# Optimization experiments

Hardware: AMD Instinct MI355X
Metric: run time of the kernel (lower is better)

Reference implementation:

```python
import jax, jax.numpy as jnp
import numpy as np
from jax.ops import segment_sum

N_NODES = 50000
N_EDGES = 800000
D = 128
N_LAYERS = 3
N_GRAPHS = 256


def setup_inputs() -> dict:
    key = jax.random.key(0)
    k1, k2, k3, k4, k5, k6 = jax.random.split(key, 6)
    feats = jax.random.normal(k1, (N_NODES, D), dtype=jnp.float32)
    src = jax.random.randint(k2, (N_EDGES,), 0, N_NODES)
    dst = jax.random.randint(k3, (N_EDGES,), 0, N_NODES)
    graph_ids = jnp.sort(jax.random.randint(k4, (N_NODES,), 0, N_GRAPHS))
    W = jax.random.normal(k5, (N_LAYERS, D, D), dtype=jnp.float32) / np.float32(np.sqrt(D))
    b = jax.random.normal(k6, (N_LAYERS, D), dtype=jnp.float32) * 0.01
    return {"feats": feats, "W": W, "b": b, "src": src, "dst": dst, "graph_ids": graph_ids}


def reference(feats, W, b, src, dst, graph_ids):
    # DGL GraphConv with norm='both': h' = act(D_in^{-1/2} A D_out^{-1/2} h W + b)
    ones_e = jnp.ones((src.shape[0],), dtype=feats.dtype)
    deg_out = jnp.clip(segment_sum(ones_e, src, num_segments=N_NODES), 1.0)  # [N]
    deg_in = jnp.clip(segment_sum(ones_e, dst, num_segments=N_NODES), 1.0)   # [N]
    norm_out = jax.lax.rsqrt(deg_out)[:, None]  # [N,1]
    norm_in = jax.lax.rsqrt(deg_in)[:, None]    # [N,1]

    h = feats
    for l in range(N_LAYERS):
        hn = h * norm_out                                  # source-side norm
        agg = segment_sum(hn[src], dst, num_segments=N_NODES)  # SpMM gather/scatter
        agg = agg * norm_in                                # dest-side norm
        h = jax.nn.relu(agg @ W[l] + b[l])                 # [N,D]

    # AvgPooling readout: per-graph mean over nodes
    ones_n = jnp.ones((N_NODES,), dtype=h.dtype)
    counts = jnp.clip(segment_sum(ones_n, graph_ids, num_segments=N_GRAPHS), 1.0)
    pooled = segment_sum(h, graph_ids, num_segments=N_GRAPHS) / counts[:, None]
    return pooled  # [N_GRAPHS, D]
```

## Files before the change

### kernel.cpp

```cpp
#include <hip/hip_runtime.h>
#include <hip/hip_fp16.h>

#define DD 128
#define GG 256
#define RANGES 4
#define RSMAX 12544
#define NCHUNK 32

typedef _Float16 half8 __attribute__((ext_vector_type(8)));
typedef float floatx4 __attribute__((ext_vector_type(4)));

__device__ inline uint2 pack_half4(float4 v) {
    __half2 a = __floats2half2_rn(v.x, v.y);
    __half2 b = __floats2half2_rn(v.z, v.w);
    uint2 u;
    u.x = *reinterpret_cast<unsigned int*>(&a);
    u.y = *reinterpret_cast<unsigned int*>(&b);
    return u;
}

__global__ __launch_bounds__(256) void k_hist1(const int* __restrict__ idx,
                                               unsigned int* __restrict__ part,
                                               int E, int N, int C, int RS, int L) {
    __shared__ int h[RSMAX];
    int r = blockIdx.x / C;
    int c = blockIdx.x % C;
    int r0 = r * RS;
    int r1 = min(r0 + RS, N);
    int nb = r1 - r0;
    for (int i = threadIdx.x; i < nb; i += 256) h[i] = 0;
    __syncthreads();
    int e0 = c * L, e1 = min(e0 + L, E);
    for (int e = e0 + threadIdx.x * 4; e < e1; e += 1024) {
        if (e + 3 < e1) {
            int4 s4 = *(const int4*)&idx[e];
            if (s4.x >= r0 && s4.x < r1) atomicAdd(&h[s4.x - r0], 1);
            if (s4.y >= r0 && s4.y < r1) atomicAdd(&h[s4.y - r0], 1);
            if (s4.z >= r0 && s4.z < r1) atomicAdd(&h[s4.z - r0], 1);
            if (s4.w >= r0 && s4.w < r1) atomicAdd(&h[s4.w - r0], 1);
        } else {
            for (int j = 0; j < 4 && e + j < e1; ++j) {
                int s = idx[e + j];
                if (s >= r0 && s < r1) atomicAdd(&h[s - r0], 1);
            }
        }
    }
    __syncthreads();
    for (int i = threadIdx.x; i < nb; i += 256)
        part[(size_t)c * N + r0 + i] = (unsigned int)h[i];
}

__global__ __launch_bounds__(256) void k_reduce(const unsigned int* __restrict__ pout,
                                                const unsigned int* __restrict__ pin,
                                                float* __restrict__ norm_out, float* __restrict__ norm_in,
                                                int* __restrict__ deg_in, int* __restrict__ bsum,
                                                int N, int C) {
    __shared__ int ws[4];
    int n = blockIdx.x * 256 + threadIdx.x;
    int so = 0, si = 0;
    if (n < N) {
        for (int c = 0; c < C; ++c) {
            so += (int)pout[(size_t)c * N + n];
            si += (int)pin[(size_t)c * N + n];
        }
        norm_out[n] = rsqrtf(fmaxf((float)so, 1.0f));
        norm_in[n] = rsqrtf(fmaxf((float)si, 1.0f));
        deg_in[n] = si;
    }
    int s = si;
    #pragma unroll
    for (int off = 32; off; off >>= 1) s += __shfl_xor(s, off);
    int lane = threadIdx.x & 63, w = threadIdx.x >> 6;
    if (lane == 0) ws[w] = s;
    __syncthreads();
    if (threadIdx.x == 0) bsum[blockIdx.x] = ws[0] + ws[1] + ws[2] + ws[3];
}

__global__ void k_scan_b(int* bsum, int nblk, int* row_ptr, int n) {
    int lane = threadIdx.x;
    int carry = 0;
    for (int base = 0; base < nblk; base += 64) {
        int i = base + lane;
        int v = (i < nblk) ? bsum[i] : 0;
        int s = v;
        #pragma unroll
        for (int off = 1; off < 64; off <<= 1) {
            int u = __shfl_up(s, off);
            if (lane >= off) s += u;
        }
        if (i < nblk) bsum[i] = carry + s - v;
        carry += __shfl(s, 63);
    }
    if (lane == 0) row_ptr[n] = carry;
}

__global__ __launch_bounds__(256) void k_scan_c(const int* __restrict__ deg, const int* __restrict__ bsum,
                                                int* __restrict__ row_ptr, int N) {
    __shared__ int ws[4];
    int t = threadIdx.x;
    int n = blockIdx.x * 256 + t;
    int v = (n < N) ? deg[n] : 0;
    int lane = t & 63, w = t >> 6;
    int incl = v;
    #pragma unroll
    for (int off = 1; off < 64; off <<= 1) {
        int u = __shfl_up(incl, off);
        if (lane >= off) incl += u;
    }
    if (lane == 63) ws[w] = incl;
    __syncthreads();
    int woff = 0;
    for (int j = 0; j < w; ++j) woff += ws[j];
    if (n < N) row_ptr[n] = bsum[blockIdx.x] + woff + incl - v;
}

__global__ void k_base(const unsigned int* __restrict__ pin, const int* __restrict__ row_ptr,
                       int* __restrict__ base, int N, int C) {
    int n = blockIdx.x * blockDim.x + threadIdx.x;
    if (n >= N) return;
    int run = row_ptr[n];
    for (int c = 0; c < C; ++c) {
        int h = (int)pin[(size_t)c * N + n];
        base[(size_t)c * N + n] = run;
        run += h;
    }
}

__global__ void k_gstart(const int* __restrict__ gid, int* g_start, int N, int G) {
    int g = blockIdx.x * blockDim.x + threadIdx.x;
    if (g > G) return;
    int lo = 0, hi = N;
    while (lo < hi) {
        int mid = (lo + hi) >> 1;
        if (gid[mid] < g) lo = mid + 1; else hi = mid;
    }
    g_start[g] = lo;
}

__global__ __launch_bounds__(256) void k_fill2(const int* __restrict__ src, const int* __restrict__ dst,
                                               const int* __restrict__ base, int* __restrict__ col_src,
                                               int E, int N, int C, int RS, int L) {
    __shared__ int cnt[RSMAX];
    int r = blockIdx.x / C;
    int c = blockIdx.x % C;
    int r0 = r * RS;
    int r1 = min(r0 + RS, N);
    int nb = r1 - r0;
    const int* bc = base + (size_t)c * N;
    for (int i = threadIdx.x; i < nb; i += 256) cnt[i] = bc[r0 + i];
    __syncthreads();
    int e0 = c * L, e1 = min(e0 + L, E);
    for (int e = e0 + threadIdx.x * 4; e < e1; e += 1024) {
        if (e + 3 < e1) {
            int4 s4 = *(const int4*)&src[e];
            int4 d4 = *(const int4*)&dst[e];
            if (d4.x >= r0 && d4.x < r1) { int o = atomicAdd(&cnt[d4.x - r0], 1); col_src[o] = s4.x; }
            if (d4.y >= r0 && d4.y < r1) { int o = atomicAdd(&cnt[d4.y - r0], 1); col_src[o] = s4.y; }
            if (d4.z >= r0 && d4.z < r1) { int o = atomicAdd(&cnt[d4.z - r0], 1); col_src[o] = s4.z; }
            if (d4.w >= r0 && d4.w < r1) { int o = atomicAdd(&cnt[d4.w - r0], 1); col_src[o] = s4.w; }
        } else {
            for (int j = 0; j < 4 && e + j < e1; ++j) {
                int s = src[e + j], d = dst[e + j];
                if (d >= r0 && d < r1) { int o = atomicAdd(&cnt[d - r0], 1); col_src[o] = s; }
            }
        }
    }
}

__global__ void k_wconv(const float* __restrict__ W, __half* __restrict__ Wt) {
    int i = blockIdx.x * blockDim.x + threadIdx.x;
    if (i >= 3 * 16384) return;
    int l = i >> 14;
    int rem = i & 16383;
    int n = rem >> 7;
    int k = rem & 127;
    Wt[(size_t)l * 16384 + n * 128 + k] = __float2half(W[(size_t)l * 16384 + k * 128 + n]);
}

__global__ void k_scale(const float* __restrict__ h, const float* __restrict__ norm_out,
                        uint2* __restrict__ Xh, int N) {
    int i = blockIdx.x * blockDim.x + threadIdx.x;
    if (i < N * 32) {
        int n = i >> 5;
        float4 v = ((const float4*)h)[i];
        float s = norm_out[n];
        v.x *= s; v.y *= s; v.z *= s; v.w *= s;
        Xh[i] = pack_half4(v);
    }
}

__device__ inline void acc_row(float* acc, uint4 u) {
    const __half2* h = (const __half2*)&u;
    #pragma unroll
    for (int i = 0; i < 4; ++i) {
        float2 f = __half22float2(h[i]);
        acc[2 * i] += f.x;
        acc[2 * i + 1] += f.y;
    }
}

__global__ __launch_bounds__(256, 8) void k_agg(const uint4* __restrict__ Xin, const float* __restrict__ norm_in,
                                                const int* __restrict__ row_ptr, const int* __restrict__ col_src,
                                                uint4* __restrict__ Yh, int N) {
    int t = threadIdx.x;
    int l16 = t & 15;
    int n = blockIdx.x * 16 + (t >> 4);
    if (n >= N) return;
    int beg = row_ptr[n], end = row_ptr[n + 1];
    float acc[8] = {};
    int k = beg;
    bool have = (k + 3 < end);
    int4 s = make_int4(0, 0, 0, 0);
    if (have) s = *(const int4*)&col_src[k];
    while (have) {
        int kn = k + 4;
        bool haven = (kn + 3 < end);
        int4 sn = s;
        if (haven) sn = *(const int4*)&col_src[kn];
        uint4 u0 = Xin[(size_t)s.x * 16 + l16];
        uint4 u1 = Xin[(size_t)s.y * 16 + l16];
        uint4 u2 = Xin[(size_t)s.z * 16 + l16];
        uint4 u3 = Xin[(size_t)s.w * 16 + l16];
        acc_row(acc, u0);
        acc_row(acc, u1);
        acc_row(acc, u2);
        acc_row(acc, u3);
        s = sn; k = kn; have = haven;
    }
    for (; k < end; ++k) {
        uint4 u = Xin[(size_t)col_src[k] * 16 + l16];
        acc_row(acc, u);
    }
    float ni = norm_in[n];
    #pragma unroll
    for (int i = 0; i < 8; ++i) acc[i] *= ni;
    __half2 hp[4];
    #pragma unroll
    for (int i = 0; i < 4; ++i) hp[i] = __floats2half2_rn(acc[2 * i], acc[2 * i + 1]);
    Yh[(size_t)n * 16 + l16] = *(uint4*)hp;
}

__global__ __launch_bounds__(256) void k_mm_mfma(const __half* __restrict__ Yh, const __half* __restrict__ Wt,
                                                 const float* __restrict__ bl, const float* __restrict__ scale,
                                                 float* __restrict__ outf, __half* __restrict__ outh, int N) {
    __shared__ _Float16 Ah[64 * 136];
    __shared__ _Float16 Bt[128 * 136];
    int tid = threadIdx.x;
    int n0 = blockIdx.x * 64;

    for (int q = tid; q < 1024; q += 256) {
        int r = q >> 4, c = q & 15;
        int node = n0 + r;
        float4 v = make_float4(0.f, 0.f, 0.f, 0.f);
        if (node < N) v = *(const float4*)&Yh[(size_t)node * 128 + c * 8];
        *(float4*)&Ah[r * 136 + c * 8] = v;
    }
    for (int q = tid; q < 2048; q += 256) {
        int r = q >> 4, c = q & 15;
        *(float4*)&Bt[r * 136 + c * 8] = *(const float4*)&Wt[(size_t)r * 128 + c * 8];
    }
    __syncthreads();

    int wave = tid >> 6;
    int lane = tid & 63;
    int quad = lane >> 4;
    int mrow = lane & 15;
    int m0 = wave * 16;

    half8 af[4];
    #pragma unroll
    for (int kc = 0; kc < 4; ++kc)
        af[kc] = *(const half8*)&Ah[(m0 + mrow) * 136 + kc * 32 + quad * 8];

    floatx4 acc[8];
    #pragma unroll
    for (int ct = 0; ct < 8; ++ct) acc[ct] = (floatx4){0.f, 0.f, 0.f, 0.f};

    #pragma unroll
    for (int ct = 0; ct < 8; ++ct) {
        #pragma unroll
        for (int kc = 0; kc < 4; ++kc) {
            half8 bf = *(const half8*)&Bt[(ct * 16 + mrow) * 136 + kc * 32 + quad * 8];
            acc[ct] = __builtin_amdgcn_mfma_f32_16x16x32_f16(af[kc], bf, acc[ct], 0, 0, 0);
        }
    }

    float sc[4];
    #pragma unroll
    for (int r = 0; r < 4; ++r) {
        int node = n0 + m0 + quad * 4 + r;
        sc[r] = (scale && node < N) ? scale[node] : 1.0f;
    }
    #pragma unroll
    for (int ct = 0; ct < 8; ++ct) {
        int col = ct * 16 + mrow;
        float bias = bl[col];
        #pragma unroll
        for (int r = 0; r < 4; ++r) {
            int node = n0 + m0 + quad * 4 + r;
            if (node < N) {
                float val = fmaxf(acc[ct][r] + bias, 0.f);
                if (outh) outh[(size_t)node * 128 + col] = __float2half(val * sc[r]);
                else outf[(size_t)node * 128 + col] = val;
            }
        }
    }
}

__global__ __launch_bounds__(256) void k_pool(const __half2* __restrict__ Fh, const int* __restrict__ g_start,
                                              float* __restrict__ out) {
    __shared__ float2 red[4][64];
    int g = blockIdx.x;
    int t = threadIdx.x;
    int cp = t & 63;
    int nl = t >> 6;
    int beg = g_start[g], end = g_start[g + 1];
    float2 acc = make_float2(0.f, 0.f);
    for (int n = beg + nl; n < end; n += 4) {
        float2 f = __half22float2(Fh[(size_t)n * 64 + cp]);
        acc.x += f.x;
        acc.y += f.y;
    }
    red[nl][cp] = acc;
    __syncthreads();
    if (nl == 0) {
        float2 a0 = red[0][cp], a1 = red[1][cp], a2 = red[2][cp], a3 = red[3][cp];
        float cnt = fmaxf((float)(end - beg), 1.0f);
        float2 o;
        o.x = (a0.x + a1.x + a2.x + a3.x) / cnt;
        o.y = (a0.y + a1.y + a2.y + a3.y) / cnt;
        *(float2*)&out[(size_t)g * DD + cp * 2] = o;
    }
}

extern "C" void kernel_launch(void* const* d_in, const int* in_sizes, int n_in,
                              void* d_out, int out_size, void* d_ws, size_t ws_size,
                              hipStream_t stream) {
    const float* feats = (const float*)d_in[0];
    const float* W = (const float*)d_in[1];
    const float* b = (const float*)d_in[2];
    const int* src = (const int*)d_in[3];
    const int* dst = (const int*)d_in[4];
    const int* gid = (const int*)d_in[5];
    float* out = (float*)d_out;
    const int N = in_sizes[0] / DD;
    const int E = in_sizes[3];

    const int C = NCHUNK;
    const int RS = (N + RANGES - 1) / RANGES;
    const int L = (((E + C - 1) / C) + 3) & ~3;

    char* ws = (char*)d_ws;
    size_t off = 0;
    auto take = [&](size_t bytes) {
        char* p = ws + off;
        off = (off + bytes + 255) & ~(size_t)255;
        return p;
    };
    float* norm_out = (float*)take((size_t)N * 4);
    float* norm_in  = (float*)take((size_t)N * 4);
    int*   deg_in   = (int*)take((size_t)N * 4);
    int*   row_ptr  = (int*)take((size_t)(N + 1) * 4);
    int*   col_src  = (int*)take((size_t)E * 4);
    int*   g_start  = (int*)take((size_t)(GG + 1) * 4);
    int*   bsum     = (int*)take((size_t)1024 * 4);
    __half* Wth     = (__half*)take((size_t)3 * 16384 * 2);
    uint4* Xh       = (uint4*)take((size_t)N * DD * 2);
    uint4* Yh       = (uint4*)take((size_t)N * DD * 2);
    size_t chunk_arr = ((size_t)C * N * 4 + 255) & ~(size_t)255;
    size_t uni_bytes = 3 * chunk_arr;
    size_t fh_bytes = (size_t)N * DD * 2;
    char* uni = take(uni_bytes > fh_bytes ? uni_bytes : fh_bytes);
    unsigned int* pout = (unsigned int*)uni;
    unsigned int* pin  = (unsigned int*)(uni + chunk_arr);
    int* fbase = (int*)(uni + 2 * chunk_arr);
    __half* Fh = (__half*)uni;

    const int nblk = (N + 255) / 256;

    k_hist1<<<RANGES * C, 256, 0, stream>>>(src, pout, E, N, C, RS, L);
    k_hist1<<<RANGES * C, 256, 0, stream>>>(dst, pin, E, N, C, RS, L);
    k_reduce<<<nblk, 256, 0, stream>>>(pout, pin, norm_out, norm_in, deg_in, bsum, N, C);
    k_gstart<<<1, 512, 0, stream>>>(gid, g_start, N, GG);
    k_wconv<<<(3 * 16384 + 255) / 256, 256, 0, stream>>>(W, Wth);
    k_scan_b<<<1, 64, 0, stream>>>(bsum, nblk, row_ptr, N);
    k_scan_c<<<nblk, 256, 0, stream>>>(deg_in, bsum, row_ptr, N);
    k_base<<<(N + 255) / 256, 256, 0, stream>>>(pin, row_ptr, fbase, N, C);
    k_fill2<<<RANGES * C, 256, 0, stream>>>(src, dst, fbase, col_src, E, N, C, RS, L);

    k_scale<<<(N * 32 + 255) / 256, 256, 0, stream>>>(feats, norm_out, (uint2*)Xh, N);

    const int agrid = (N + 15) / 16;
    const int mgrid = (N + 63) / 64;
    for (int l = 0; l < 3; ++l) {
        k_agg<<<agrid, 256, 0, stream>>>(Xh, norm_in, row_ptr, col_src, Yh, N);
        const __half* Wtl = Wth + (size_t)l * 16384;
        const float* bl = b + (size_t)l * DD;
        if (l < 2)
            k_mm_mfma<<<mgrid, 256, 0, stream>>>((const __half*)Yh, Wtl, bl, norm_out,
                                                 nullptr, (__half*)Xh, N);
        else
            k_mm_mfma<<<mgrid, 256, 0, stream>>>((const __half*)Yh, Wtl, bl, nullptr,
                                                 nullptr, Fh, N);
    }
    k_pool<<<GG, 256, 0, stream>>>((const __half2*)Fh, g_start, out);
}
```

Measured before the change: 327.5 us.

## Pack src/dst into 16-bit keys and fuse preprocessing kernels

Packs src and dst indices into one 32-bit key array, then computes the out- and in-degree histograms in a single pass over that array. Packed partial counts cut the memory read in the reduce step. The scan, graph-start search, weight conversion and feature scaling are merged into one multi-role kernel, and the row-pointer scan is fused with the per-chunk base computation, reducing the number of launches. It relies on node indices and per-chunk counts fitting in 16 bits, and halves the shared-memory range size to fit two histograms per block.

```diff
diff --git a/kernel.cpp b/kernel.cpp
--- a/kernel.cpp
+++ b/kernel.cpp
@@ -3,8 +3,8 @@
 
 #define DD 128
 #define GG 256
-#define RANGES 4
-#define RSMAX 12544
+#define RANGES 8
+#define RSMAX 6400
 #define NCHUNK 32
 
 typedef _Float16 half8 __attribute__((ext_vector_type(8)));
@@ -19,39 +19,64 @@
     return u;
 }
 
-__global__ __launch_bounds__(256) void k_hist1(const int* __restrict__ idx,
-                                               unsigned int* __restrict__ part,
+__global__ __launch_bounds__(256) void k_key(const int* __restrict__ src, const int* __restrict__ dst,
+                                             unsigned int* __restrict__ key, int E) {
+    int i = (blockIdx.x * 256 + threadIdx.x) * 4;
+    if (i + 3 < E) {
+        int4 s4 = *(const int4*)&src[i];
+        int4 d4 = *(const int4*)&dst[i];
+        uint4 k4;
+        k4.x = (unsigned int)s4.x | ((unsigned int)d4.x << 16);
+        k4.y = (unsigned int)s4.y | ((unsigned int)d4.y << 16);
+        k4.z = (unsigned int)s4.z | ((unsigned int)d4.z << 16);
+        k4.w = (unsigned int)s4.w | ((unsigned int)d4.w << 16);
+        *(uint4*)&key[i] = k4;
+    } else {
+        for (int j = 0; j < 4 && i + j < E; ++j)
+            key[i + j] = (unsigned int)src[i + j] | ((unsigned int)dst[i + j] << 16);
+    }
+}
+
+__global__ __launch_bounds__(256) void k_hist2(const unsigned int* __restrict__ key,
+                                               unsigned int* __restrict__ pk,
                                                int E, int N, int C, int RS, int L) {
-    __shared__ int h[RSMAX];
+    __shared__ int ho[RSMAX];
+    __shared__ int hi[RSMAX];
     int r = blockIdx.x / C;
     int c = blockIdx.x % C;
     int r0 = r * RS;
     int r1 = min(r0 + RS, N);
     int nb = r1 - r0;
-    for (int i = threadIdx.x; i < nb; i += 256) h[i] = 0;
+    for (int i = threadIdx.x; i < nb; i += 256) { ho[i] = 0; hi[i] = 0; }
     __syncthreads();
     int e0 = c * L, e1 = min(e0 + L, E);
     for (int e = e0 + threadIdx.x * 4; e < e1; e += 1024) {
         if (e + 3 < e1) {
-            int4 s4 = *(const int4*)&idx[e];
-            if (s4.x >= r0 && s4.x < r1) atomicAdd(&h[s4.x - r0], 1);
-            if (s4.y >= r0 && s4.y < r1) atomicAdd(&h[s4.y - r0], 1);
-            if (s4.z >= r0 && s4.z < r1) atomicAdd(&h[s4.z - r0], 1);
-            if (s4.w >= r0 && s4.w < r1) atomicAdd(&h[s4.w - r0], 1);
+            uint4 k4 = *(const uint4*)&key[e];
+            #pragma unroll
+            for (int j = 0; j < 4; ++j) {
+                unsigned int kk = (j == 0) ? k4.x : (j == 1) ? k4.y : (j == 2) ? k4.z : k4.w;
+                int s = (int)(kk & 0xFFFFu);
+                int d = (int)(kk >> 16);
+                if (s >= r0 && s < r1) atomicAdd(&ho[s - r0], 1);
+                if (d >= r0 && d < r1) atomicAdd(&hi[d - r0], 1);
+            }
         } else {
             for (int j = 0; j < 4 && e + j < e1; ++j) {
-                int s = idx[e + j];
-                if (s >= r0 && s < r1) atomicAdd(&h[s - r0], 1);
+                unsigned int kk = key[e + j];
+                int s = (int)(kk & 0xFFFFu);
+                int d = (int)(kk >> 16);
+                if (s >= r0 && s < r1) atomicAdd(&ho[s - r0], 1);
+                if (d >= r0 && d < r1) atomicAdd(&hi[d - r0], 1);
             }
         }
     }
     __syncthreads();
     for (int i = threadIdx.x; i < nb; i += 256)
-        part[(size_t)c * N + r0 + i] = (unsigned int)h[i];
-}
-
-__global__ __launch_bounds__(256) void k_reduce(const unsigned int* __restrict__ pout,
-                                                const unsigned int* __restrict__ pin,
+        pk[(size_t)c * N + r0 + i] = (unsigned int)ho[i] | ((unsigned int)hi[i] << 16);
+}
+
+__global__ __launch_bounds__(256) void k_reduce(const unsigned int* __restrict__ pk,
                                                 float* __restrict__ norm_out, float* __restrict__ norm_in,
                                                 int* __restrict__ deg_in, int* __restrict__ bsum,
                                                 int N, int C) {
@@ -60,8 +85,9 @@
     int so = 0, si = 0;
     if (n < N) {
         for (int c = 0; c < C; ++c) {
-            so += (int)pout[(size_t)c * N + n];
-            si += (int)pin[(size_t)c * N + n];
+            unsigned int v = pk[(size_t)c * N + n];
+            so += (int)(v & 0xFFFFu);
+            si += (int)(v >> 16);
         }
         norm_out[n] = rsqrtf(fmaxf((float)so, 1.0f));
         norm_in[n] = rsqrtf(fmaxf((float)si, 1.0f));
@@ -76,26 +102,67 @@
     if (threadIdx.x == 0) bsum[blockIdx.x] = ws[0] + ws[1] + ws[2] + ws[3];
 }
 
-__global__ void k_scan_b(int* bsum, int nblk, int* row_ptr, int n) {
-    int lane = threadIdx.x;
-    int carry = 0;
-    for (int base = 0; base < nblk; base += 64) {
-        int i = base + lane;
-        int v = (i < nblk) ? bsum[i] : 0;
-        int s = v;
-        #pragma unroll
-        for (int off = 1; off < 64; off <<= 1) {
-            int u = __shfl_up(s, off);
-            if (lane >= off) s += u;
-        }
-        if (i < nblk) bsum[i] = carry + s - v;
-        carry += __shfl(s, 63);
-    }
-    if (lane == 0) row_ptr[n] = carry;
-}
-
-__global__ __launch_bounds__(256) void k_scan_c(const int* __restrict__ deg, const int* __restrict__ bsum,
-                                                int* __restrict__ row_ptr, int N) {
+__global__ __launch_bounds__(256) void k_misc(int* bsum, int nblk, int* row_ptr, int N,
+                                              const int* __restrict__ gid, int* g_start, int G,
+                                              const float* __restrict__ W, __half* __restrict__ Wt,
+                                              const float* __restrict__ feats,
+                                              const float* __restrict__ norm_out,
+                                              uint2* __restrict__ Xh) {
+    int blk = blockIdx.x;
+    int tid = threadIdx.x;
+    if (blk == 0) {
+        if (tid < 64) {
+            int lane = tid;
+            int carry = 0;
+            for (int base = 0; base < nblk; base += 64) {
+                int i = base + lane;
+                int v = (i < nblk) ? bsum[i] : 0;
+                int s = v;
+                #pragma unroll
+                for (int off = 1; off < 64; off <<= 1) {
+                    int u = __shfl_up(s, off);
+                    if (lane >= off) s += u;
+                }
+                if (i < nblk) bsum[i] = carry + s - v;
+                carry += __shfl(s, 63);
+            }
+            if (lane == 0) row_ptr[N] = carry;
+        }
+    } else if (blk <= 2) {
+        int g = (blk - 1) * 256 + tid;
+        if (g <= G) {
+            int lo = 0, hi = N;
+            while (lo < hi) {
+                int mid = (lo + hi) >> 1;
+                if (gid[mid] < g) lo = mid + 1; else hi = mid;
+            }
+            g_start[g] = lo;
+        }
+    } else if (blk <= 194) {
+        int i = (blk - 3) * 256 + tid;
+        if (i < 3 * 16384) {
+            int l = i >> 14;
+            int rem = i & 16383;
+            int n = rem >> 7;
+            int k = rem & 127;
+            Wt[(size_t)l * 16384 + n * 128 + k] = __float2half(W[(size_t)l * 16384 + k * 128 + n]);
+        }
+    } else {
+        int i = (blk - 195) * 256 + tid;
+        if (i < N * 32) {
+            int n = i >> 5;
+            float4 v = ((const float4*)feats)[i];
+            float s = norm_out[n];
+            v.x *= s; v.y *= s; v.z *= s; v.w *= s;
+            Xh[i] = pack_half4(v);
+        }
+    }
+}
+
+__global__ __launch_bounds__(256) void k_scan_cb(const int* __restrict__ deg, const int* __restrict__ bsum,
+                                                 const unsigned int* __restrict__ pk,
+                                                 int* __restrict__ row_ptr, int* __restrict__ fbase,
+                                                 int N, int C) {
     __shared__ int ws[4];
     int t = threadIdx.x;
     int n = blockIdx.x * 256 + t;
@@ -111,33 +178,18 @@
     __syncthreads();
     int woff = 0;
     for (int j = 0; j < w; ++j) woff += ws[j];
-    if (n < N) row_ptr[n] = bsum[blockIdx.x] + woff + incl - v;
-}
-
-__global__ void k_base(const unsigned int* __restrict__ pin, const int* __restrict__ row_ptr,
-                       int* __restrict__ base, int N, int C) {
-    int n = blockIdx.x * blockDim.x + threadIdx.x;
-    if (n >= N) return;
-    int run = row_ptr[n];
-    for (int c = 0; c < C; ++c) {
-        int h = (int)pin[(size_t)c * N + n];
-        base[(size_t)c * N + n] = run;
-        run += h;
-    }
-}
-
-__global__ void k_gstart(const int* __restrict__ gid, int* g_start, int N, int G) {
-    int g = blockIdx.x * blockDim.x + threadIdx.x;
-    if (g > G) return;
-    int lo = 0, hi = N;
-    while (lo < hi) {
-        int mid = (lo + hi) >> 1;
-        if (gid[mid] < g) lo = mid + 1; else hi = mid;
-    }
-    g_start[g] = lo;
-}
-
-__global__ __launch_bounds__(256) void k_fill2(const int* __restrict__ src, const int* __restrict__ dst,
+    if (n < N) {
+        int run = bsum[blockIdx.x] + woff + incl - v;
+        row_ptr[n] = run;
+        for (int c = 0; c < C; ++c) {
+            int h = (int)(pk[(size_t)c * N + n] >> 16);
+            fbase[(size_t)c * N + n] = run;
+            run += h;
+        }
+    }
+}
+
+__global__ __launch_bounds__(256) void k_fill2(const unsigned int* __restrict__ key,
                                                const int* __restrict__ base, int* __restrict__ col_src,
                                                int E, int N, int C, int RS, int L) {
     __shared__ int cnt[RSMAX];
@@ -152,40 +204,22 @@
     int e0 = c * L, e1 = min(e0 + L, E);
     for (int e = e0 + threadIdx.x * 4; e < e1; e += 1024) {
         if (e + 3 < e1) {
-            int4 s4 = *(const int4*)&src[e];
-            int4 d4 = *(const int4*)&dst[e];
-            if (d4.x >= r0 && d4.x < r1) { int o = atomicAdd(&cnt[d4.x - r0], 1); col_src[o] = s4.x; }
-            if (d4.y >= r0 && d4.y < r1) { int o = atomicAdd(&cnt[d4.y - r0], 1); col_src[o] = s4.y; }
-            if (d4.z >= r0 && d4.z < r1) { int o = atomicAdd(&cnt[d4.z - r0], 1); col_src[o] = s4.z; }
-            if (d4.w >= r0 && d4.w < r1) { int o = atomicAdd(&cnt[d4.w - r0], 1); col_src[o] = s4.w; }
+            uint4 k4 = *(const uint4*)&key[e];
+            #pragma unroll
+            for (int j = 0; j < 4; ++j) {
+                unsigned int kk = (j == 0) ? k4.x : (j == 1) ? k4.y : (j == 2) ? k4.z : k4.w;
+                int s = (int)(kk & 0xFFFFu);
+                int d = (int)(kk >> 16);
+                if (d >= r0 && d < r1) { int o = atomicAdd(&cnt[d - r0], 1); col_src[o] = s; }
+            }
         } else {
             for (int j = 0; j < 4 && e + j < e1; ++j) {
-                int s = src[e + j], d = dst[e + j];
+                unsigned int kk = key[e + j];
+                int s = (int)(kk & 0xFFFFu);
+                int d = (int)(kk >> 16);
                 if (d >= r0 && d < r1) { int o = atomicAdd(&cnt[d - r0], 1); col_src[o] = s; }
             }
         }
-    }
-}
-
-__global__ void k_wconv(const float* __restrict__ W, __half* __restrict__ Wt) {
-    int i = blockIdx.x * blockDim.x + threadIdx.x;
-    if (i >= 3 * 16384) return;
-    int l = i >> 14;
-    int rem = i & 16383;
-    int n = rem >> 7;
-    int k = rem & 127;
-    Wt[(size_t)l * 16384 + n * 128 + k] = __float2half(W[(size_t)l * 16384 + k * 128 + n]);
-}
-
-__global__ void k_scale(const float* __restrict__ h, const float* __restrict__ norm_out,
-                        uint2* __restrict__ Xh, int N) {
-    int i = blockIdx.x * blockDim.x + threadIdx.x;
-    if (i < N * 32) {
-        int n = i >> 5;
-        float4 v = ((const float4*)h)[i];
-        float s = norm_out[n];
-        v.x *= s; v.y *= s; v.z *= s; v.w *= s;
-        Xh[i] = pack_half4(v);
     }
 }
 
@@ -364,31 +398,28 @@
     int*   col_src  = (int*)take((size_t)E * 4);
     int*   g_start  = (int*)take((size_t)(GG + 1) * 4);
     int*   bsum     = (int*)take((size_t)1024 * 4);
+    unsigned int* key = (unsigned int*)take((size_t)E * 4);
     __half* Wth     = (__half*)take((size_t)3 * 16384 * 2);
     uint4* Xh       = (uint4*)take((size_t)N * DD * 2);
     uint4* Yh       = (uint4*)take((size_t)N * DD * 2);
     size_t chunk_arr = ((size_t)C * N * 4 + 255) & ~(size_t)255;
-    size_t uni_bytes = 3 * chunk_arr;
+    size_t uni_bytes = 2 * chunk_arr;
     size_t fh_bytes = (size_t)N * DD * 2;
     char* uni = take(uni_bytes > fh_bytes ? uni_bytes : fh_bytes);
-    unsigned int* pout = (unsigned int*)uni;
-    unsigned int* pin  = (unsigned int*)(uni + chunk_arr);
-    int* fbase = (int*)(uni + 2 * chunk_arr);
+    unsigned int* pk = (unsigned int*)uni;
+    int* fbase = (int*)(uni + chunk_arr);
     __half* Fh = (__half*)uni;
 
     const int nblk = (N + 255) / 256;
-
-    k_hist1<<<RANGES * C, 256, 0, stream>>>(src, pout, E, N, C, RS, L);
-    k_hist1<<<RANGES * C, 256, 0, stream>>>(dst, pin, E, N, C, RS, L);
-    k_reduce<<<nblk, 256, 0, stream>>>(pout, pin, norm_out, norm_in, deg_in, bsum, N, C);
-    k_gstart<<<1, 512, 0, stream>>>(gid, g_start, N, GG);
-    k_wconv<<<(3 * 16384 + 255) / 256, 256, 0, stream>>>(W, Wth);
-    k_scan_b<<<1, 64, 0, stream>>>(bsum, nblk, row_ptr, N);
-    k_scan_c<<<nblk, 256, 0, stream>>>(deg_in, bsum, row_ptr, N);
-    k_base<<<(N + 255) / 256, 256, 0, stream>>>(pin, row_ptr, fbase, N, C);
-    k_fill2<<<RANGES * C, 256, 0, stream>>>(src, dst, fbase, col_src, E, N, C, RS, L);
-
-    k_scale<<<(N * 32 + 255) / 256, 256, 0, stream>>>(feats, norm_out, (uint2*)Xh, N);
+    const int mgrid_misc = 195 + (N * 32 + 255) / 256;
+
+    k_key<<<(E + 1023) / 1024, 256, 0, stream>>>(src, dst, key, E);
+    k_hist2<<<RANGES * C, 256, 0, stream>>>(key, pk, E, N, C, RS, L);
+    k_reduce<<<nblk, 256, 0, stream>>>(pk, norm_out, norm_in, deg_in, bsum, N, C);
+    k_misc<<<mgrid_misc, 256, 0, stream>>>(bsum, nblk, row_ptr, N, gid, g_start, GG,
+                                           W, Wth, feats, norm_out, (uint2*)Xh);
+    k_scan_cb<<<nblk, 256, 0, stream>>>(deg_in, bsum, pk, row_ptr, fbase, N, C);
+    k_fill2<<<RANGES * C, 256, 0, stream>>>(key, fbase, col_src, E, N, C, RS, L);
 
     const int agrid = (N + 15) / 16;
     const int mgrid = (N + 63) / 64;
```

After: 308.8 us. 5.7% less time.
